# Optimization experiments

Measured on AMD Instinct MI355X. Metric: run time of the kernel, lower is better.

The kernel has to match this reference:

```python
import jax, jax.numpy as jnp
import numpy as np

N, E, G = 50000, 800000, 128
IN, HID, OUT, H = 38, 64, 128, 4
NEG_SLOPE = 0.2
EPS = 1e-16


def setup_inputs() -> dict:
    key = jax.random.key(0)
    ks = jax.random.split(key, 16)
    s = 0.05
    inp = {
        "x": jax.random.normal(ks[0], (N, IN), jnp.float32),
        "edge_index": jax.random.randint(ks[1], (2, E), 0, N),
        "batch": jnp.sort(jax.random.randint(ks[2], (N,), 0, G)),
        # GATv2 layer 1: in=38 -> heads=4, C=64 (concat -> 256)
        "Wl1": jax.random.normal(ks[3], (IN, H * HID), jnp.float32) * s,
        "bl1": jnp.zeros((H * HID,), jnp.float32),
        "Wr1": jax.random.normal(ks[4], (IN, H * HID), jnp.float32) * s,
        "br1": jnp.zeros((H * HID,), jnp.float32),
        "att1": jax.random.normal(ks[5], (H, HID), jnp.float32) * s,
        "bias1": jnp.zeros((H * HID,), jnp.float32),
        # GATv2 layer 2: in=256 -> heads=1, C=128
        "Wl2": jax.random.normal(ks[6], (H * HID, OUT), jnp.float32) * s,
        "bl2": jnp.zeros((OUT,), jnp.float32),
        "Wr2": jax.random.normal(ks[7], (H * HID, OUT), jnp.float32) * s,
        "br2": jnp.zeros((OUT,), jnp.float32),
        "att2": jax.random.normal(ks[8], (1, OUT), jnp.float32) * s,
        "bias2": jnp.zeros((OUT,), jnp.float32),
    }
    return inp


def gatv2(x, src, dst, Wl, bl, Wr, br, att, bias, heads, C):
    n = x.shape[0]
    xl = (x @ Wl + bl).reshape(n, heads, C)  # source transform
    xr = (x @ Wr + br).reshape(n, heads, C)  # target transform
    e = jax.nn.leaky_relu(xl[src] + xr[dst], NEG_SLOPE)  # [E', H, C]
    logits = jnp.einsum("ehc,hc->eh", e, att)
    # segment softmax over incoming edges of each destination node
    m = jax.ops.segment_max(logits, dst, num_segments=n)
    p = jnp.exp(logits - m[dst])
    denom = jax.ops.segment_sum(p, dst, num_segments=n)
    alpha = p / (denom[dst] + EPS)  # [E', H]
    msg = xl[src] * alpha[..., None]
    out = jax.ops.segment_sum(msg, dst, num_segments=n)  # [N, H, C]
    return out.reshape(n, heads * C) + bias


def reference(x, edge_index, batch, Wl1, bl1, Wr1, br1, att1, bias1,
              Wl2, bl2, Wr2, br2, att2, bias2):
    n = x.shape[0]
    loops = jnp.arange(n, dtype=edge_index.dtype)
    src = jnp.concatenate([edge_index[0], loops])  # add_self_loops (PyG default)
    dst = jnp.concatenate([edge_index[1], loops])
    h = jax.nn.relu(gatv2(x, src, dst, Wl1, bl1, Wr1, br1, att1, bias1, H, HID))
    # dropout is identity at inference
    h = jax.nn.relu(gatv2(h, src, dst, Wl2, bl2, Wr2, br2, att2, bias2, 1, OUT))
    # global mean pool over graphs
    sums = jax.ops.segment_sum(h, batch, num_segments=G)
    counts = jax.ops.segment_sum(jnp.ones((n,), h.dtype), batch, num_segments=G)
    return sums / jnp.maximum(counts, 1.0)[:, None]
```

## Files before the change

### kernel.cpp

```cpp
#include <hip/hip_runtime.h>
#include <hip/hip_bf16.h>
#include <limits.h>

#define N_NODES 50000
#define N_EDGES 800000
#define TOT_E   (N_EDGES + N_NODES)
#define IN_F    38
#define HIDC    64
#define NH      4
#define F1      256
#define F2      128
#define NGRAPH  128
#define NEG_SLOPE 0.2f
#define EPS_A   1e-16f

typedef __hip_bfloat16 bf16;
typedef unsigned char fp8_t;
typedef __attribute__((ext_vector_type(8))) short short8;
typedef __attribute__((ext_vector_type(16))) float f32x16;
typedef __attribute__((ext_vector_type(2))) float f2;

constexpr size_t al256(size_t x) { return (x + 255) & ~(size_t)255; }

#define P_WL1   0
#define P_BL1   (P_WL1 + IN_F * F1)
#define P_WR1   (P_BL1 + F1)
#define P_BR1   (P_WR1 + IN_F * F1)
#define P_ATT1  (P_BR1 + F1)
#define P_BIAS1 (P_ATT1 + F1)
#define P_WL2   (P_BIAS1 + F1)
#define P_BL2   (P_WL2 + F1 * F2)
#define P_WR2   (P_BL2 + F2)
#define P_BR2   (P_WR2 + F1 * F2)
#define P_ATT2  (P_BR2 + F2)
#define P_BIAS2 (P_ATT2 + F2)
#define P_TOTAL (P_BIAS2 + F2)

constexpr size_t OFF_PAR  = 256;
constexpr size_t OFF_XL1  = OFF_PAR + al256((size_t)P_TOTAL * 4);
constexpr size_t OFF_XR1  = OFF_XL1 + al256((size_t)N_NODES * F1 * 2);
constexpr size_t OFF_H    = OFF_XR1 + al256((size_t)N_NODES * F1 * 2);
constexpr size_t OFF_XL2  = OFF_H   + al256((size_t)N_NODES * F1 * 2);
constexpr size_t OFF_XR2  = OFF_XL2 + al256((size_t)N_NODES * F2 * 2);
constexpr size_t OFF_CNT  = OFF_XR2 + al256((size_t)N_NODES * F2 * 2);
constexpr size_t OFF_OFFS = OFF_CNT + al256((size_t)N_NODES * 4);
constexpr size_t OFF_CSR  = OFF_OFFS+ al256((size_t)(N_NODES + 1) * 4);
constexpr size_t OFF_GS   = OFF_CSR + al256((size_t)TOT_E * 4);
constexpr size_t OFF_GE   = OFF_GS  + al256((size_t)NGRAPH * 4);
constexpr size_t OFF_WT1  = OFF_GE  + al256((size_t)NGRAPH * 4);
constexpr size_t OFF_WT2  = OFF_WT1 + al256((size_t)512 * 64 * 2);
constexpr size_t OFF_BS   = OFF_WT2 + al256((size_t)256 * 256 * 2);
constexpr size_t OFF_PSUM = OFF_BS  + al256(64 * 4);
constexpr size_t OFF_RANK = OFF_PSUM+ al256((size_t)NGRAPH * F2 * 4);
constexpr size_t OFF_H2   = OFF_XL1;
constexpr size_t OFF_XB   = OFF_H;

#define SCAN_BLKS 49
#define GBLK 1563
#define SBL  831

__device__ __forceinline__ void unpack8bf2(uint4 q, f2* f) {
  unsigned v[4] = {q.x, q.y, q.z, q.w};
#pragma unroll
  for (int i = 0; i < 4; i++) {
    f2 t;
    t.x = __uint_as_float(v[i] << 16);
    t.y = __uint_as_float(v[i] & 0xffff0000u);
    f[i] = t;
  }
}

__device__ __forceinline__ void load8bf2(const bf16* __restrict__ p, f2* f) {
  unpack8bf2(*(const uint4*)p, f);
}

__device__ __forceinline__ void unpack8fp8(uint2 q, f2* f) {
  f[0] = __builtin_amdgcn_cvt_pk_f32_fp8(q.x, false);
  f[1] = __builtin_amdgcn_cvt_pk_f32_fp8(q.x, true);
  f[2] = __builtin_amdgcn_cvt_pk_f32_fp8(q.y, false);
  f[3] = __builtin_amdgcn_cvt_pk_f32_fp8(q.y, true);
}

__device__ __forceinline__ fp8_t f32_to_fp8(float v) {
  return (fp8_t)(__builtin_amdgcn_cvt_pk_fp8_f32(v, v, 0, false) & 0xFF);
}

__device__ __forceinline__ f2 lrelu2(f2 s) {
  f2 as;
  as.x = __uint_as_float(__float_as_uint(s.x) & 0x7fffffffu);
  as.y = __uint_as_float(__float_as_uint(s.y) & 0x7fffffffu);
  return 0.6f * s + 0.4f * as;
}

__device__ __forceinline__ int detect_f32_wave(const void* __restrict__ x) {
  const unsigned short* u = (const unsigned short*)x;
  unsigned short b = u[threadIdx.x & 63];
  int e = (b >> 7) & 0xFF;
  unsigned long long m = __ballot(!((e == 0) || (e >= 96 && e <= 158)));
  return __popcll(m) > 8;
}

#define B_CVT  338
#define B_XP   1563
#define B_W1   128
#define B_W2   256
#define B_BND  196
#define B_CNT  831

struct PrepArgs {
  const void* x;
  const void* src[12];
  const int* ei;
  const int* batch;
};

__global__ __launch_bounds__(256) void prep_k(
    PrepArgs a, float* __restrict__ par, bf16* __restrict__ xb,
    bf16* __restrict__ wt1, bf16* __restrict__ wt2,
    int* __restrict__ gs, int* __restrict__ ge, int* __restrict__ cnt,
    int* __restrict__ rank) {
  int b = blockIdx.x;
  const int tid = threadIdx.x;

  if (b < B_CVT) {
    const int flag = detect_f32_wave(a.x);
    int idx = b * 256 + tid;
    const void* p; int base;
    if      (idx < P_BL1)  { p = a.src[0];  base = P_WL1; }
    else if (idx < P_WR1)  { p = a.src[1];  base = P_BL1; }
    else if (idx < P_BR1)  { p = a.src[2];  base = P_WR1; }
    else if (idx < P_ATT1) { p = a.src[3];  base = P_BR1; }
    else if (idx < P_BIAS1){ p = a.src[4];  base = P_ATT1; }
    else if (idx < P_WL2)  { p = a.src[5];  base = P_BIAS1; }
    else if (idx < P_BL2)  { p = a.src[6];  base = P_WL2; }
    else if (idx < P_WR2)  { p = a.src[7];  base = P_BL2; }
    else if (idx < P_BR2)  { p = a.src[8];  base = P_WR2; }
    else if (idx < P_ATT2) { p = a.src[9];  base = P_BR2; }
    else if (idx < P_BIAS2){ p = a.src[10]; base = P_ATT2; }
    else                   { p = a.src[11]; base = P_BIAS2; }
    int li = idx - base;
    par[idx] = flag ? ((const float*)p)[li] : (float)((const bf16*)p)[li];
    return;
  }
  b -= B_CVT;
  if (b < B_XP) {
    const int flag = detect_f32_wave(a.x);
    int gid = b * 256 + tid;
    int n = gid >> 3, k0 = (gid & 7) * 8;
    float v[8];
#pragma unroll
    for (int j = 0; j < 8; j++) {
      int k = k0 + j;
      v[j] = 0.f;
      if (k < IN_F) {
        int idx = n * IN_F + k;
        v[j] = flag ? ((const float*)a.x)[idx] : (float)((const bf16*)a.x)[idx];
      }
    }
    __align__(16) bf16 ob[8];
#pragma unroll
    for (int j = 0; j < 8; j++) ob[j] = (bf16)v[j];
    *(uint4*)(xb + (size_t)n * 64 + k0) = *(uint4*)ob;
    return;
  }
  b -= B_XP;
  if (b < B_W1) {
    const int flag = detect_f32_wave(a.x);
    int i = b * 256 + tid;
    int n = i >> 6, k = i & 63;
    float v = 0.f;
    if (k < IN_F) {
      const void* W = (n < F1) ? a.src[0] : a.src[2];
      int col = (n < F1) ? n : n - F1;
      int idx = k * F1 + col;
      v = flag ? ((const float*)W)[idx] : (float)((const bf16*)W)[idx];
    }
    wt1[i] = (bf16)v;
    return;
  }
  b -= B_W1;
  if (b < B_W2) {
    const int flag = detect_f32_wave(a.x);
    int i = b * 256 + tid;
    int n = i >> 8, k = i & 255;
    const void* W = (n < F2) ? a.src[6] : a.src[8];
    int col = (n < F2) ? n : n - F2;
    int idx = k * F2 + col;
    float v = flag ? ((const float*)W)[idx] : (float)((const bf16*)W)[idx];
    wt2[i] = (bf16)v;
    return;
  }
  b -= B_W2;
  if (b < B_BND) {
    int n = b * 256 + tid;
    if (n >= N_NODES) return;
    int bb = a.batch[n];
    if (n == 0) gs[bb] = 0;
    else {
      int bp = a.batch[n - 1];
      if (bp != bb) { gs[bb] = n; ge[bp] = n - 1; }
    }
    if (n == N_NODES - 1) ge[bb] = N_NODES - 1;
    return;
  }
  b -= B_BND;
  {
    int base = b * 1024 + tid;
    int dstv[4]; bool val[4];
#pragma unroll
    for (int i = 0; i < 4; i++) {
      int e = base + i * 256;
      val[i] = e < TOT_E;
      dstv[i] = 0;
      if (val[i])
        dstv[i] = (e < N_EDGES) ? a.ei[N_EDGES + e] : (e - N_EDGES);
    }
#pragma unroll
    for (int i = 0; i < 4; i++) {
      int e = base + i * 256;
      if (val[i]) rank[e] = atomicAdd(&cnt[dstv[i]], 1);
    }
  }
}

__global__ __launch_bounds__(256) void gemm1_scatter_k(
    const bf16* __restrict__ xb, const bf16* __restrict__ wt1,
    const float* __restrict__ par,
    fp8_t* __restrict__ xl1, bf16* __restrict__ xr1,
    const int* __restrict__ ei, const int* __restrict__ offs,
    const int* __restrict__ rank, int* __restrict__ csr) {
  if (blockIdx.x >= GBLK) {
    int base = (blockIdx.x - GBLK) * 1024 + threadIdx.x;
#pragma unroll
    for (int i = 0; i < 4; i++) {
      int e = base + i * 256;
      if (e >= TOT_E) continue;
      int src, dst;
      if (e < N_EDGES) { src = ei[e]; dst = ei[N_EDGES + e]; }
      else             { src = dst = e - N_EDGES; }
      csr[offs[dst] + rank[e]] = src;
    }
    return;
  }
  const int w = threadIdx.x >> 6, lane = threadIdx.x & 63;
  const int m0 = blockIdx.x * 32;
  const int colbase = w * 128;
  const int lm = lane & 31;
  const int kh = lane >> 5;

  int arow = m0 + lm; if (arow >= N_NODES) arow = N_NODES - 1;
  short8 afr[4];
#pragma unroll
  for (int kk = 0; kk < 4; kk++)
    afr[kk] = *(const short8*)(xb + (size_t)arow * 64 + kk * 16 + kh * 8);

  f32x16 acc[4] = {};
#pragma unroll
  for (int t = 0; t < 4; t++) {
    int n = colbase + t * 32 + lm;
#pragma unroll
    for (int kk = 0; kk < 4; kk++) {
      short8 b = *(const short8*)(wt1 + (size_t)n * 64 + kk * 16 + kh * 8);
      acc[t] = __builtin_amdgcn_mfma_f32_32x32x16_bf16(afr[kk], b, acc[t], 0, 0, 0);
    }
  }

#pragma unroll
  for (int t = 0; t < 4; t++) {
    int col = colbase + t * 32 + lm;
    if (col < F1) {
      float bv = par[P_BL1 + col];
#pragma unroll
      for (int reg = 0; reg < 16; reg++) {
        int row = m0 + (reg & 3) + 8 * (reg >> 2) + 4 * kh;
        if (row < N_NODES)
          xl1[(size_t)row * F1 + col] = f32_to_fp8(acc[t][reg] + bv);
      }
    } else {
      int c = col - F1;
      float bv = par[P_BR1 + c];
#pragma unroll
      for (int reg = 0; reg < 16; reg++) {
        int row = m0 + (reg & 3) + 8 * (reg >> 2) + 4 * kh;
        if (row < N_NODES)
          xr1[(size_t)row * F1 + c] = (bf16)(acc[t][reg] + bv);
      }
    }
  }
}

__global__ __launch_bounds__(256) void gemm2_mfma_k(
    const bf16* __restrict__ h, const bf16* __restrict__ wt2,
    const float* __restrict__ par,
    fp8_t* __restrict__ xl2, bf16* __restrict__ xr2) {
  const int w = threadIdx.x >> 6, lane = threadIdx.x & 63;
  const int m0 = blockIdx.x * 32;
  const int colbase = w * 64;
  const int lm = lane & 31;
  const int kh = lane >> 5;

  int arow = m0 + lm; if (arow >= N_NODES) arow = N_NODES - 1;
  const bf16* hrow = h + (size_t)arow * F1 + kh * 8;

  f32x16 acc[2] = {};
#pragma unroll
  for (int kk = 0; kk < 16; kk++) {
    short8 a = *(const short8*)(hrow + kk * 16);
#pragma unroll
    for (int t = 0; t < 2; t++) {
      int n = colbase + t * 32 + lm;
      short8 b = *(const short8*)(wt2 + (size_t)n * 256 + kk * 16 + kh * 8);
      acc[t] = __builtin_amdgcn_mfma_f32_32x32x16_bf16(a, b, acc[t], 0, 0, 0);
    }
  }

#pragma unroll
  for (int t = 0; t < 2; t++) {
    int col = colbase + t * 32 + lm;
    if (col < F2) {
      float bv = par[P_BL2 + col];
#pragma unroll
      for (int reg = 0; reg < 16; reg++) {
        int row = m0 + (reg & 3) + 8 * (reg >> 2) + 4 * kh;
        if (row < N_NODES)
          xl2[(size_t)row * F2 + col] = f32_to_fp8(acc[t][reg] + bv);
      }
    } else {
      int c = col - F2;
      float bv = par[P_BR2 + c];
#pragma unroll
      for (int reg = 0; reg < 16; reg++) {
        int row = m0 + (reg & 3) + 8 * (reg >> 2) + 4 * kh;
        if (row < N_NODES)
          xr2[(size_t)row * F2 + c] = (bf16)(acc[t][reg] + bv);
      }
    }
  }
}

__global__ __launch_bounds__(1024) void scan_a(const int* __restrict__ cnt,
                                               int* __restrict__ offs,
                                               int* __restrict__ bsum) {
  __shared__ int wsum[16];
  const int t = threadIdx.x;
  const int lane = t & 63, w = t >> 6;
  int idx = blockIdx.x * 1024 + t;
  int v = (idx < N_NODES) ? cnt[idx] : 0;
  int s = v;
#pragma unroll
  for (int off = 1; off < 64; off <<= 1) {
    int u = __shfl_up(s, off, 64);
    if (lane >= off) s += u;
  }
  if (lane == 63) wsum[w] = s;
  __syncthreads();
  int prefix = 0;
  for (int i = 0; i < w; i++) prefix += wsum[i];
  if (idx < N_NODES) offs[idx] = prefix + s - v;
  if (t == 1023) bsum[blockIdx.x] = prefix + s;
}

__global__ void scan_c(const int* __restrict__ bsum, int* __restrict__ offs) {
  const int t = threadIdx.x;
  const int grp = blockIdx.x >> 2;
  __shared__ int sboff;
  if (t < 64) {
    int v = (t < SCAN_BLKS) ? bsum[t] : 0;
    int s = v;
#pragma unroll
    for (int off = 1; off < 64; off <<= 1) {
      int u = __shfl_up(s, off, 64);
      if (t >= off) s += u;
    }
    if (t == grp) sboff = s - v;
  }
  __syncthreads();
  int idx = blockIdx.x * 256 + t;
  if (idx < N_NODES) offs[idx] += sboff;
  if (blockIdx.x == 0 && t == 0) offs[N_NODES] = TOT_E;
}

__global__ __launch_bounds__(256, 4) void agg1_k(
    const fp8_t* __restrict__ xl1, const bf16* __restrict__ xr1,
    const float* __restrict__ par,
    const int* __restrict__ offs, const int* __restrict__ csr,
    bf16* __restrict__ hout) {
  const int dst = blockIdx.x * 4 + (threadIdx.x >> 6);
  if (dst >= N_NODES) return;
  const int lane = threadIdx.x & 63;
  const int g = lane >> 5;
  const int sl = lane & 31;
  const int chb = sl * 8;

  f2 r2[4], a2[4];
  load8bf2(xr1 + (size_t)dst * F1 + chb, r2);
  {
    float4 aa = *(const float4*)(par + P_ATT1 + chb);
    float4 ab = *(const float4*)(par + P_ATT1 + chb + 4);
    a2[0].x = aa.x; a2[0].y = aa.y; a2[1].x = aa.z; a2[1].y = aa.w;
    a2[2].x = ab.x; a2[2].y = ab.y; a2[3].x = ab.z; a2[3].y = ab.w;
  }

  const int e0 = offs[dst], e1 = offs[dst + 1];
  const f2 zf2 = {0.f, 0.f};
  f2 acc2[4];
#pragma unroll
  for (int j = 0; j < 4; j++) acc2[j] = zf2;
  float denom = 0.f;

  const uint2 zq = {0, 0};
  int e = e0 + g;
  bool valid = e < e1;
  uint2 q = valid ? *(const uint2*)(xl1 + (size_t)csr[e] * F1 + chb) : zq;

  for (int base = e0; base < e1; base += 2) {
    const uint2 qc = q;
    const bool vc = valid;
    e += 2;
    valid = e < e1;
    q = valid ? *(const uint2*)(xl1 + (size_t)csr[e] * F1 + chb) : zq;

    f2 v2[4];
    unpack8fp8(qc, v2);
    f2 lt2 = zf2;
#pragma unroll
    for (int j = 0; j < 4; j++)
      lt2 = lrelu2(v2[j] + r2[j]) * a2[j] + lt2;
    float lt = vc ? (lt2.x + lt2.y) : -1e30f;
    lt += __shfl_xor(lt, 1, 64);
    lt += __shfl_xor(lt, 2, 64);
    lt += __shfl_xor(lt, 4, 64);
    float p = __expf(fminf(lt, 60.f));
    denom += p;
    f2 pv; pv.x = p; pv.y = p;
#pragma unroll
    for (int j = 0; j < 4; j++) acc2[j] = pv * v2[j] + acc2[j];
  }

  denom += __shfl_xor(denom, 32, 64);
#pragma unroll
  for (int j = 0; j < 4; j++) {
    acc2[j].x += __shfl_xor(acc2[j].x, 32, 64);
    acc2[j].y += __shfl_xor(acc2[j].y, 32, 64);
  }

  if (g == 0) {
    float inv = 1.f / (denom + EPS_A);
    __align__(16) bf16 ob[8];
#pragma unroll
    for (int j = 0; j < 4; j++) {
      float o0 = fmaxf(acc2[j].x * inv + par[P_BIAS1 + chb + 2*j],     0.f);
      float o1 = fmaxf(acc2[j].y * inv + par[P_BIAS1 + chb + 2*j + 1], 0.f);
      ob[2*j] = (bf16)o0; ob[2*j+1] = (bf16)o1;
    }
    *(uint4*)(hout + (size_t)dst * F1 + chb) = *(uint4*)ob;
  }
}

__global__ __launch_bounds__(256, 4) void agg2_k(
    const fp8_t* __restrict__ xl2, const bf16* __restrict__ xr2,
    const float* __restrict__ par,
    const int* __restrict__ offs, const int* __restrict__ csr,
    bf16* __restrict__ h2) {
  const int dst = blockIdx.x * 4 + (threadIdx.x >> 6);
  if (dst >= N_NODES) return;
  const int lane = threadIdx.x & 63;
  const int g = lane >> 4;
  const int sl = lane & 15;
  const int chb = sl * 8;

  f2 r2[4], a2[4];
  load8bf2(xr2 + (size_t)dst * F2 + chb, r2);
  {
    float4 aa = *(const float4*)(par + P_ATT2 + chb);
    float4 ab = *(const float4*)(par + P_ATT2 + chb + 4);
    a2[0].x = aa.x; a2[0].y = aa.y; a2[1].x = aa.z; a2[1].y = aa.w;
    a2[2].x = ab.x; a2[2].y = ab.y; a2[3].x = ab.z; a2[3].y = ab.w;
  }

  const int e0 = offs[dst], e1 = offs[dst + 1];
  const f2 zf2 = {0.f, 0.f};
  f2 acc2[4];
#pragma unroll
  for (int j = 0; j < 4; j++) acc2[j] = zf2;
  float denom = 0.f;

  const uint2 zq = {0, 0};
  int e = e0 + g;
  bool valid = e < e1;
  uint2 q = valid ? *(const uint2*)(xl2 + (size_t)csr[e] * F2 + chb) : zq;

  for (int base = e0; base < e1; base += 4) {
    const uint2 qc = q;
    const bool vc = valid;
    e += 4;
    valid = e < e1;
    q = valid ? *(const uint2*)(xl2 + (size_t)csr[e] * F2 + chb) : zq;

    f2 v2[4];
    unpack8fp8(qc, v2);
    f2 lt2 = zf2;
#pragma unroll
    for (int j = 0; j < 4; j++)
      lt2 = lrelu2(v2[j] + r2[j]) * a2[j] + lt2;
    float lt = vc ? (lt2.x + lt2.y) : -1e30f;
    lt += __shfl_xor(lt, 1, 64);
    lt += __shfl_xor(lt, 2, 64);
    lt += __shfl_xor(lt, 4, 64);
    lt += __shfl_xor(lt, 8, 64);
    float p = __expf(fminf(lt, 60.f));
    denom += p;
    f2 pv; pv.x = p; pv.y = p;
#pragma unroll
    for (int j = 0; j < 4; j++) acc2[j] = pv * v2[j] + acc2[j];
  }

#pragma unroll
  for (int m = 16; m <= 32; m <<= 1) {
    denom += __shfl_xor(denom, m, 64);
#pragma unroll
    for (int j = 0; j < 4; j++) {
      acc2[j].x += __shfl_xor(acc2[j].x, m, 64);
      acc2[j].y += __shfl_xor(acc2[j].y, m, 64);
    }
  }

  if (g == 0) {
    float inv = 1.f / (denom + EPS_A);
    __align__(16) bf16 ob[8];
#pragma unroll
    for (int j = 0; j < 4; j++) {
      float o0 = fmaxf(acc2[j].x * inv + par[P_BIAS2 + chb + 2*j],     0.f);
      float o1 = fmaxf(acc2[j].y * inv + par[P_BIAS2 + chb + 2*j + 1], 0.f);
      ob[2*j] = (bf16)o0; ob[2*j+1] = (bf16)o1;
    }
    *(uint4*)(h2 + (size_t)dst * F2 + chb) = *(uint4*)ob;
  }
}

__global__ __launch_bounds__(256) void poolp_k(
    const bf16* __restrict__ h2, const int* __restrict__ gs,
    const int* __restrict__ ge, float* __restrict__ psum) {
  const int g = blockIdx.x >> 3, slice = blockIdx.x & 7;
  const int t = threadIdx.x;
  const int c = t & 127, half = t >> 7;
  int s = gs[g], e = ge[g];
  if (s < 0 || e < s) return;
  float sum = 0.f;
  for (int n = s + slice * 2 + half; n <= e; n += 16)
    sum += (float)h2[(size_t)n * F2 + c];
  atomicAdd(&psum[g * F2 + c], sum);
}

__global__ void poolf_k(const float* __restrict__ psum,
                        const int* __restrict__ gs, const int* __restrict__ ge,
                        const void* __restrict__ x, void* __restrict__ out) {
  int i = blockIdx.x * 256 + threadIdx.x;
  if (i >= NGRAPH * F2) return;
  const int flag = detect_f32_wave(x);
  int g = i >> 7;
  int s = gs[g], e = ge[g];
  float cnt = (s >= 0 && e >= s) ? (float)(e - s + 1) : 1.f;
  float v = psum[i] / cnt;
  if (flag) ((float*)out)[i] = v;
  else      ((bf16*)out)[i] = (bf16)v;
}

extern "C" void kernel_launch(void* const* d_in, const int* in_sizes, int n_in,
                              void* d_out, int out_size, void* d_ws, size_t ws_size,
                              hipStream_t stream) {
  (void)in_sizes; (void)n_in; (void)out_size; (void)ws_size;
  const void* x     = d_in[0];
  const int*  ei    = (const int*)d_in[1];
  const int*  batch = (const int*)d_in[2];

  char* ws = (char*)d_ws;
  float* par  = (float*)(ws + OFF_PAR);
  fp8_t* xl1 = (fp8_t*)(ws + OFF_XL1);
  bf16* xr1 = (bf16*)(ws + OFF_XR1);
  bf16* h   = (bf16*)(ws + OFF_H);
  fp8_t* xl2 = (fp8_t*)(ws + OFF_XL2);
  bf16* xr2 = (bf16*)(ws + OFF_XR2);
  bf16* h2  = (bf16*)(ws + OFF_H2);
  bf16* xb  = (bf16*)(ws + OFF_XB);
  bf16* wt1 = (bf16*)(ws + OFF_WT1);
  bf16* wt2 = (bf16*)(ws + OFF_WT2);
  int* cnt    = (int*)(ws + OFF_CNT);
  int* offs   = (int*)(ws + OFF_OFFS);
  int* csr    = (int*)(ws + OFF_CSR);
  int* gs     = (int*)(ws + OFF_GS);
  int* ge     = (int*)(ws + OFF_GE);
  int* bsum   = (int*)(ws + OFF_BS);
  float* psum = (float*)(ws + OFF_PSUM);
  int* rank   = (int*)(ws + OFF_RANK);

  hipMemsetAsync(cnt, 0, (size_t)N_NODES * 4, stream);
  hipMemsetAsync(gs, 0xFF, (size_t)(OFF_WT1 - OFF_GS), stream);
  hipMemsetAsync(psum, 0, (size_t)NGRAPH * F2 * 4, stream);

  PrepArgs pa;
  pa.x = x; pa.ei = ei; pa.batch = batch;
  for (int i = 0; i < 12; i++) pa.src[i] = d_in[3 + i];
  const int prep_blocks = B_CVT + B_XP + B_W1 + B_W2 + B_BND + B_CNT;
  prep_k<<<prep_blocks, 256, 0, stream>>>(pa, par, xb, wt1, wt2, gs, ge, cnt, rank);

  scan_a<<<SCAN_BLKS, 1024, 0, stream>>>(cnt, offs, bsum);
  scan_c<<<(N_NODES + 255) / 256, 256, 0, stream>>>(bsum, offs);

  gemm1_scatter_k<<<GBLK + SBL, 256, 0, stream>>>(xb, wt1, par, xl1, xr1,
                                                  ei, offs, rank, csr);
  agg1_k<<<(N_NODES + 3) / 4, 256, 0, stream>>>(xl1, xr1, par, offs, csr, h);
  gemm2_mfma_k<<<GBLK, 256, 0, stream>>>(h, wt2, par, xl2, xr2);
  agg2_k<<<(N_NODES + 3) / 4, 256, 0, stream>>>(xl2, xr2, par, offs, csr, h2);
  poolp_k<<<NGRAPH * 8, 256, 0, stream>>>(h2, gs, ge, psum);
  poolf_k<<<(NGRAPH * F2 + 255) / 256, 256, 0, stream>>>(psum, gs, ge, x, d_out);
}
```

Baseline: 322.4 us.

## Stage GEMM epilogues through LDS for coalesced stores; merge workspace memsets

Both GEMM kernels now write their fp8 xl and bf16 xr outputs into shared memory first, then copy them to global memory as coalesced 16-byte row stores. Previously each lane did scattered byte or short stores per MFMA register. Separately, the workspace is rearranged so cnt, gs, ge and psum sit next to each other and can be cleared with one zero memset instead of three. To allow zero-init, gs and ge are re-encoded with a +1 bias and an exclusive end, adding a __syncthreads and LDS use to the GEMMs.

Result: no change. 318.4 us (-1.2%).

```diff
diff --git a/kernel.cpp b/kernel.cpp
--- a/kernel.cpp
+++ b/kernel.cpp
@@ -43,15 +43,16 @@
 constexpr size_t OFF_XL2  = OFF_H   + al256((size_t)N_NODES * F1 * 2);
 constexpr size_t OFF_XR2  = OFF_XL2 + al256((size_t)N_NODES * F2 * 2);
 constexpr size_t OFF_CNT  = OFF_XR2 + al256((size_t)N_NODES * F2 * 2);
-constexpr size_t OFF_OFFS = OFF_CNT + al256((size_t)N_NODES * 4);
+constexpr size_t OFF_GS   = OFF_CNT + al256((size_t)N_NODES * 4);
+constexpr size_t OFF_GE   = OFF_GS  + al256((size_t)NGRAPH * 4);
+constexpr size_t OFF_PSUM = OFF_GE  + al256((size_t)NGRAPH * 4);
+constexpr size_t OFF_ZEND = OFF_PSUM+ al256((size_t)NGRAPH * F2 * 4);
+constexpr size_t OFF_OFFS = OFF_ZEND;
 constexpr size_t OFF_CSR  = OFF_OFFS+ al256((size_t)(N_NODES + 1) * 4);
-constexpr size_t OFF_GS   = OFF_CSR + al256((size_t)TOT_E * 4);
-constexpr size_t OFF_GE   = OFF_GS  + al256((size_t)NGRAPH * 4);
-constexpr size_t OFF_WT1  = OFF_GE  + al256((size_t)NGRAPH * 4);
+constexpr size_t OFF_WT1  = OFF_CSR + al256((size_t)TOT_E * 4);
 constexpr size_t OFF_WT2  = OFF_WT1 + al256((size_t)512 * 64 * 2);
 constexpr size_t OFF_BS   = OFF_WT2 + al256((size_t)256 * 256 * 2);
-constexpr size_t OFF_PSUM = OFF_BS  + al256(64 * 4);
-constexpr size_t OFF_RANK = OFF_PSUM+ al256((size_t)NGRAPH * F2 * 4);
+constexpr size_t OFF_RANK = OFF_BS  + al256(64 * 4);
 constexpr size_t OFF_H2   = OFF_XL1;
 constexpr size_t OFF_XB   = OFF_H;
 
@@ -195,12 +196,12 @@
     int n = b * 256 + tid;
     if (n >= N_NODES) return;
     int bb = a.batch[n];
-    if (n == 0) gs[bb] = 0;
+    if (n == 0) gs[bb] = 1;
     else {
       int bp = a.batch[n - 1];
-      if (bp != bb) { gs[bb] = n; ge[bp] = n - 1; }
-    }
-    if (n == N_NODES - 1) ge[bb] = N_NODES - 1;
+      if (bp != bb) { gs[bb] = n + 1; ge[bp] = n; }
+    }
+    if (n == N_NODES - 1) ge[bb] = N_NODES;
     return;
   }
   b -= B_BND;
@@ -229,6 +230,7 @@
     fp8_t* __restrict__ xl1, bf16* __restrict__ xr1,
     const int* __restrict__ ei, const int* __restrict__ offs,
     const int* __restrict__ rank, int* __restrict__ csr) {
+  __shared__ char lds[24576];
   if (blockIdx.x >= GBLK) {
     int base = (blockIdx.x - GBLK) * 1024 + threadIdx.x;
 #pragma unroll
@@ -265,27 +267,50 @@
     }
   }
 
-#pragma unroll
-  for (int t = 0; t < 4; t++) {
-    int col = colbase + t * 32 + lm;
-    if (col < F1) {
+  char* lds8  = lds;
+  bf16* lds16 = (bf16*)(lds + 8192);
+  if (w < 2) {
+#pragma unroll
+    for (int t = 0; t < 4; t++) {
+      int col = colbase + t * 32 + lm;
       float bv = par[P_BL1 + col];
 #pragma unroll
       for (int reg = 0; reg < 16; reg++) {
-        int row = m0 + (reg & 3) + 8 * (reg >> 2) + 4 * kh;
-        if (row < N_NODES)
-          xl1[(size_t)row * F1 + col] = f32_to_fp8(acc[t][reg] + bv);
+        int rl = (reg & 3) + 8 * (reg >> 2) + 4 * kh;
+        lds8[rl * 256 + col] = f32_to_fp8(acc[t][reg] + bv);
       }
-    } else {
-      int c = col - F1;
+    }
+  } else {
+#pragma unroll
+    for (int t = 0; t < 4; t++) {
+      int c = colbase - 256 + t * 32 + lm;
       float bv = par[P_BR1 + c];
 #pragma unroll
       for (int reg = 0; reg < 16; reg++) {
-        int row = m0 + (reg & 3) + 8 * (reg >> 2) + 4 * kh;
-        if (row < N_NODES)
-          xr1[(size_t)row * F1 + c] = (bf16)(acc[t][reg] + bv);
+        int rl = (reg & 3) + 8 * (reg >> 2) + 4 * kh;
+        lds16[rl * 256 + c] = (bf16)(acc[t][reg] + bv);
       }
     }
+  }
+  __syncthreads();
+
+  const int tid = threadIdx.x;
+#pragma unroll
+  for (int i = 0; i < 2; i++) {
+    int idx = tid + i * 256;
+    int row = idx >> 4, ck = (idx & 15) * 16;
+    int grow = m0 + row;
+    if (grow < N_NODES)
+      *(uint4*)(xl1 + (size_t)grow * F1 + ck) = *(uint4*)(lds8 + row * 256 + ck);
+  }
+#pragma unroll
+  for (int i = 0; i < 4; i++) {
+    int idx = tid + i * 256;
+    int row = idx >> 5, ck = (idx & 31) * 16;
+    int grow = m0 + row;
+    if (grow < N_NODES)
+      *(uint4*)((char*)(xr1 + (size_t)grow * F1) + ck) =
+          *(uint4*)((char*)(lds16 + row * 256) + ck);
   }
 }
 
@@ -293,6 +318,7 @@
     const bf16* __restrict__ h, const bf16* __restrict__ wt2,
     const float* __restrict__ par,
     fp8_t* __restrict__ xl2, bf16* __restrict__ xr2) {
+  __shared__ char lds[12288];
   const int w = threadIdx.x >> 6, lane = threadIdx.x & 63;
   const int m0 = blockIdx.x * 32;
   const int colbase = w * 64;
@@ -314,27 +340,48 @@
     }
   }
 
-#pragma unroll
-  for (int t = 0; t < 2; t++) {
-    int col = colbase + t * 32 + lm;
-    if (col < F2) {
+  char* lds8  = lds;
+  bf16* lds16 = (bf16*)(lds + 4096);
+  if (w < 2) {
+#pragma unroll
+    for (int t = 0; t < 2; t++) {
+      int col = colbase + t * 32 + lm;
       float bv = par[P_BL2 + col];
 #pragma unroll
       for (int reg = 0; reg < 16; reg++) {
-        int row = m0 + (reg & 3) + 8 * (reg >> 2) + 4 * kh;
-        if (row < N_NODES)
-          xl2[(size_t)row * F2 + col] = f32_to_fp8(acc[t][reg] + bv);
+        int rl = (reg & 3) + 8 * (reg >> 2) + 4 * kh;
+        lds8[rl * 128 + col] = f32_to_fp8(acc[t][reg] + bv);
       }
-    } else {
-      int c = col - F2;
+    }
+  } else {
+#pragma unroll
+    for (int t = 0; t < 2; t++) {
+      int c = colbase - 128 + t * 32 + lm;
       float bv = par[P_BR2 + c];
 #pragma unroll
       for (int reg = 0; reg < 16; reg++) {
-        int row = m0 + (reg & 3) + 8 * (reg >> 2) + 4 * kh;
-        if (row < N_NODES)
-          xr2[(size_t)row * F2 + c] = (bf16)(acc[t][reg] + bv);
+        int rl = (reg & 3) + 8 * (reg >> 2) + 4 * kh;
+        lds16[rl * 128 + c] = (bf16)(acc[t][reg] + bv);
       }
     }
+  }
+  __syncthreads();
+
+  const int tid = threadIdx.x;
+  {
+    int row = tid >> 3, ck = (tid & 7) * 16;
+    int grow = m0 + row;
+    if (grow < N_NODES)
+      *(uint4*)(xl2 + (size_t)grow * F2 + ck) = *(uint4*)(lds8 + row * 128 + ck);
+  }
+#pragma unroll
+  for (int i = 0; i < 2; i++) {
+    int idx = tid + i * 256;
+    int row = idx >> 4, ck = (idx & 15) * 16;
+    int grow = m0 + row;
+    if (grow < N_NODES)
+      *(uint4*)((char*)(xr2 + (size_t)grow * F2) + ck) =
+          *(uint4*)((char*)(lds16 + row * 128) + ck);
   }
 }
 
@@ -544,10 +591,10 @@
   const int g = blockIdx.x >> 3, slice = blockIdx.x & 7;
   const int t = threadIdx.x;
   const int c = t & 127, half = t >> 7;
-  int s = gs[g], e = ge[g];
-  if (s < 0 || e < s) return;
+  int s = gs[g] - 1, eex = ge[g];
+  if (s < 0 || eex <= s) return;
   float sum = 0.f;
-  for (int n = s + slice * 2 + half; n <= e; n += 16)
+  for (int n = s + slice * 2 + half; n < eex; n += 16)
     sum += (float)h2[(size_t)n * F2 + c];
   atomicAdd(&psum[g * F2 + c], sum);
 }
@@ -559,8 +606,8 @@
   if (i >= NGRAPH * F2) return;
   const int flag = detect_f32_wave(x);
   int g = i >> 7;
-  int s = gs[g], e = ge[g];
-  float cnt = (s >= 0 && e >= s) ? (float)(e - s + 1) : 1.f;
+  int s = gs[g] - 1, eex = ge[g];
+  float cnt = (s >= 0 && eex > s) ? (float)(eex - s) : 1.f;
   float v = psum[i] / cnt;
   if (flag) ((float*)out)[i] = v;
   else      ((bf16*)out)[i] = (bf16)v;
@@ -594,9 +641,7 @@
   float* psum = (float*)(ws + OFF_PSUM);
   int* rank   = (int*)(ws + OFF_RANK);
 
-  hipMemsetAsync(cnt, 0, (size_t)N_NODES * 4, stream);
-  hipMemsetAsync(gs, 0xFF, (size_t)(OFF_WT1 - OFF_GS), stream);
-  hipMemsetAsync(psum, 0, (size_t)NGRAPH * F2 * 4, stream);
+  hipMemsetAsync(cnt, 0, OFF_ZEND - OFF_CNT, stream);
 
   PrepArgs pa;
   pa.x = x; pa.ei = ei; pa.batch = batch;
```
